# Kernel tuning notes

Hardware: AMD Instinct MI355X
Metric: run time of the kernel (lower is better)

## Reference

```python
import jax, jax.numpy as jnp
import numpy as np

N_NODES = 100000
N_EDGES = 1600000
D_IN = 128
D_OUT = 128


def setup_inputs() -> dict:
    key = jax.random.key(0)
    k1, k2, k3, k4, k5, k6 = jax.random.split(key, 6)
    x = jax.random.normal(k1, (N_NODES, D_IN), dtype=jnp.float32)
    adj_rows = jnp.sort(jax.random.randint(k2, (N_EDGES,), 0, N_NODES, dtype=jnp.int32))
    adj_cols = jax.random.randint(k3, (N_EDGES,), 0, N_NODES, dtype=jnp.int32)
    adj_vals = jax.random.uniform(k4, (N_EDGES,), dtype=jnp.float32)
    weight = jax.random.normal(k5, (D_OUT, D_IN), dtype=jnp.float32) * (1.0 / np.sqrt(D_IN))
    bias = jax.random.normal(k6, (D_OUT,), dtype=jnp.float32) * 0.01
    return {"x": x, "adj_rows": adj_rows, "adj_cols": adj_cols,
            "adj_vals": adj_vals, "weight": weight, "bias": bias}


def reference(x, adj_rows, adj_cols, adj_vals, weight, bias):
    # w_input = inputs @ W.T  -> [N, D_OUT]
    w_input = x @ weight.T
    # SpMM: out[r] = sum_e adj_vals[e] * w_input[cols[e]] for edges with rows[e] == r
    msgs = adj_vals[:, None] * w_input[adj_cols]          # [E, D_OUT]
    agg = jax.ops.segment_sum(msgs, adj_rows, num_segments=N_NODES)
    out = jax.nn.relu(agg + bias)
    return out.astype(jnp.float32)
```

## Files before the change

### kernel.cpp

```cpp
#include <hip/hip_runtime.h>
#include <hip/hip_bf16.h>

#define D 128
#define RPW 2

typedef __attribute__((ext_vector_type(8))) short bf16x8;
typedef __attribute__((ext_vector_type(4))) float f32x4;

__device__ __forceinline__ unsigned short f2bf(float f) {
    union { float f; unsigned u; } uf{f};
    unsigned r = uf.u + 0x7fffu + ((uf.u >> 16) & 1u);
    return (unsigned short)(r >> 16);
}
__device__ __forceinline__ unsigned packcv(float a, float b) {
    __hip_bfloat162 h = __float22bfloat162_rn(make_float2(a, b));
    union { __hip_bfloat162 h; unsigned u; } c{h};
    return c.u;
}
__device__ __forceinline__ float bflo(unsigned u) {
    union { unsigned u; float f; } c{u << 16};
    return c.f;
}
__device__ __forceinline__ float bfhi(unsigned u) {
    union { unsigned u; float f; } c{u & 0xffff0000u};
    return c.f;
}
__device__ __forceinline__ int pc_col(unsigned u) { return (int)(u & 0x1FFFFu); }
__device__ __forceinline__ float pc_val(unsigned u) {
    union { unsigned u; float f; } c{(u >> 1) & 0xFFFF0000u};
    return c.f;
}

#define FMA8(A, vv, u) \
    A[0] = fmaf(vv, bflo(u.x), A[0]); A[1] = fmaf(vv, bfhi(u.x), A[1]); \
    A[2] = fmaf(vv, bflo(u.y), A[2]); A[3] = fmaf(vv, bfhi(u.y), A[3]); \
    A[4] = fmaf(vv, bflo(u.z), A[4]); A[5] = fmaf(vv, bfhi(u.z), A[5]); \
    A[6] = fmaf(vv, bflo(u.w), A[6]); A[7] = fmaf(vv, bfhi(u.w), A[7]);

__global__ __launch_bounds__(256) void build_rowptr(const int* __restrict__ rows,
                                                    const int* __restrict__ cols,
                                                    const float* __restrict__ vals,
                                                    const float* __restrict__ W,
                                                    unsigned short* __restrict__ wbf,
                                                    unsigned* __restrict__ pc,
                                                    int2* __restrict__ rowptr,
                                                    int e, int n) {
    int i = blockIdx.x * 256 + threadIdx.x;
    if (i < D * D) wbf[i] = f2bf(W[i]);
    if (i >= e) return;

    pc[i] = ((unsigned)f2bf(vals[i]) << 17) | (unsigned)cols[i];

    int r = rows[i];
    int prev = (i == 0) ? -1 : rows[i - 1];
    int next = (i == e - 1) ? n : rows[i + 1];
    if (prev != r) {
        rowptr[r].x = i;
        for (int q = prev + 1; q < r; ++q) rowptr[q] = make_int2(i, i);
    }
    if (next != r) {
        rowptr[r].y = i + 1;
        if (i == e - 1)
            for (int q = r + 1; q < n; ++q) rowptr[q] = make_int2(e, e);
    }
}

__global__ __launch_bounds__(256) void gemm_mfma(const float* __restrict__ x,
                                                 const unsigned short* __restrict__ wbf,
                                                 unsigned short* __restrict__ wi,
                                                 int nrows) {
    __shared__ __align__(16) unsigned short Ws[128 * 128];

    const int tid = threadIdx.x;
#pragma unroll
    for (int it = 0; it < 8; ++it) {
        int elem = it * 2048 + tid * 8;
        int r = elem >> 7, k = elem & 127;
        int idx = (r * 128 + k) ^ ((r & 7) << 3);
        *(uint4*)&Ws[idx] = *(const uint4*)(wbf + elem);
    }
    __syncthreads();

    const int lane = tid & 63;
    const int row0 = blockIdx.x * 128 + (tid >> 6) * 32;
    const int lrow = lane & 15;
    const int lk8 = (lane >> 4) * 8;

    bf16x8 xfrag[2][4];
#pragma unroll
    for (int xb = 0; xb < 2; ++xb)
#pragma unroll
        for (int kb = 0; kb < 4; ++kb) {
            int gr = min(row0 + xb * 16 + lrow, nrows - 1);
            const float4* p = (const float4*)(x + (size_t)gr * D + kb * 32 + lk8);
            float4 f0 = p[0], f1 = p[1];
            union { bf16x8 v; unsigned u[4]; } cv;
            cv.u[0] = packcv(f0.x, f0.y);
            cv.u[1] = packcv(f0.z, f0.w);
            cv.u[2] = packcv(f1.x, f1.y);
            cv.u[3] = packcv(f1.z, f1.w);
            xfrag[xb][kb] = cv.v;
        }

    f32x4 acc[2][8];
#pragma unroll
    for (int xb = 0; xb < 2; ++xb)
#pragma unroll
        for (int cb = 0; cb < 8; ++cb)
            acc[xb][cb] = (f32x4){0.f, 0.f, 0.f, 0.f};

#pragma unroll
    for (int cb = 0; cb < 8; ++cb) {
#pragma unroll
        for (int kb = 0; kb < 4; ++kb) {
            int wrow = cb * 16 + lrow;
            int idx = (wrow * 128 + kb * 32 + lk8) ^ ((wrow & 7) << 3);
            bf16x8 wfrag = *(const bf16x8*)&Ws[idx];
            acc[0][cb] = __builtin_amdgcn_mfma_f32_16x16x32_bf16(wfrag, xfrag[0][kb], acc[0][cb], 0, 0, 0);
            acc[1][cb] = __builtin_amdgcn_mfma_f32_16x16x32_bf16(wfrag, xfrag[1][kb], acc[1][cb], 0, 0, 0);
        }
    }

#pragma unroll
    for (int xb = 0; xb < 2; ++xb) {
        int g = row0 + xb * 16 + lrow;
        if (g < nrows) {
#pragma unroll
            for (int cb = 0; cb < 8; ++cb) {
                uint2 o;
                o.x = packcv(acc[xb][cb][0], acc[xb][cb][1]);
                o.y = packcv(acc[xb][cb][2], acc[xb][cb][3]);
                *(uint2*)(wi + (size_t)g * D + cb * 16 + (lane >> 4) * 4) = o;
            }
        }
    }
}

__global__ __launch_bounds__(256) void spmm_relu(const unsigned short* __restrict__ wi,
                                                 const int2* __restrict__ rowptr,
                                                 const unsigned* __restrict__ pc,
                                                 const float* __restrict__ bias,
                                                 float* __restrict__ out,
                                                 int n) {
    const int lane = threadIdx.x & 63;
    const int R0 = (blockIdx.x * 4 + (threadIdx.x >> 6)) * RPW;
    if (R0 >= n) return;
    const int nr = min(RPW, n - R0);

    const int2 rp = rowptr[R0 + min(lane, nr - 1)];
    const int ch = (lane & 15) * 8;
    const int sub = lane >> 4;

    float4 b0 = *(const float4*)(bias + (lane & 15) * 8);
    float4 b1 = *(const float4*)(bias + (lane & 15) * 8 + 4);

    int st = __shfl(rp.x, 0), en = __shfl(rp.y, 0);
    unsigned u = 0;
    { int idx = st + lane; if (idx < en) u = pc[idx]; }

    for (int j = 0; j < nr; ++j) {
        int st_n = 0, en_n = 0; unsigned u_n = 0;
        if (j + 1 < nr) {
            st_n = __shfl(rp.x, j + 1); en_n = __shfl(rp.y, j + 1);
            int idx = st_n + lane; if (idx < en_n) u_n = pc[idx];
        }

        float a0[8] = {0.f, 0.f, 0.f, 0.f, 0.f, 0.f, 0.f, 0.f};
        float a1[8] = {0.f, 0.f, 0.f, 0.f, 0.f, 0.f, 0.f, 0.f};

        const int cnt = min(en - st, 64);
        if (cnt > 0) {
            unsigned mA[4], mB[4];
#pragma unroll
            for (int p = 0; p < 4; ++p) {
                mA[p] = __shfl(u, sub + 4 * p);
                mB[p] = __shfl(u, 16 + sub + 4 * p);
            }
            uint4 uA[4], uB[4];
#pragma unroll
            for (int p = 0; p < 4; ++p) uA[p] = *(const uint4*)(wi + (size_t)pc_col(mA[p]) * D + ch);
#pragma unroll
            for (int p = 0; p < 4; ++p) uB[p] = *(const uint4*)(wi + (size_t)pc_col(mB[p]) * D + ch);
#pragma unroll
            for (int p = 0; p < 4; ++p) {
                FMA8(a0, pc_val(mA[p]), uA[p]);
                FMA8(a1, pc_val(mB[p]), uB[p]);
            }
            for (int E = 32; E < cnt; E += 16) {
#pragma unroll
                for (int p = 0; p < 4; ++p) {
                    unsigned m = __shfl(u, E + sub + 4 * p);
                    uint4 uq = *(const uint4*)(wi + (size_t)pc_col(m) * D + ch);
                    FMA8(a0, pc_val(m), uq);
                }
            }
        }
        for (int base = st + 64; base < en; base += 64) {
            unsigned uu = 0;
            { int idx = base + lane; if (idx < en) uu = pc[idx]; }
            const int cnt2 = min(en - base, 64);
            for (int E = 0; E < cnt2; E += 16) {
#pragma unroll
                for (int p = 0; p < 4; ++p) {
                    unsigned m = __shfl(uu, E + sub + 4 * p);
                    uint4 uq = *(const uint4*)(wi + (size_t)pc_col(m) * D + ch);
                    FMA8(a1, pc_val(m), uq);
                }
            }
        }

        float r8[8];
#pragma unroll
        for (int t = 0; t < 8; ++t) {
            float s = a0[t] + a1[t];
            s += __shfl_xor(s, 16);
            s += __shfl_xor(s, 32);
            r8[t] = s;
        }
        if (lane < 16) {
            float4 o0, o1;
            o0.x = fmaxf(r8[0] + b0.x, 0.f);
            o0.y = fmaxf(r8[1] + b0.y, 0.f);
            o0.z = fmaxf(r8[2] + b0.z, 0.f);
            o0.w = fmaxf(r8[3] + b0.w, 0.f);
            o1.x = fmaxf(r8[4] + b1.x, 0.f);
            o1.y = fmaxf(r8[5] + b1.y, 0.f);
            o1.z = fmaxf(r8[6] + b1.z, 0.f);
            o1.w = fmaxf(r8[7] + b1.w, 0.f);
            *(float4*)(out + (size_t)(R0 + j) * D + lane * 8) = o0;
            *(float4*)(out + (size_t)(R0 + j) * D + lane * 8 + 4) = o1;
        }

        st = st_n; en = en_n; u = u_n;
    }
}

extern "C" void kernel_launch(void* const* d_in, const int* in_sizes, int n_in,
                              void* d_out, int out_size, void* d_ws, size_t ws_size,
                              hipStream_t stream) {
    const float* x        = (const float*)d_in[0];
    const int*   adj_rows = (const int*)d_in[1];
    const int*   adj_cols = (const int*)d_in[2];
    const float* adj_vals = (const float*)d_in[3];
    const float* weight   = (const float*)d_in[4];
    const float* bias     = (const float*)d_in[5];
    float*       out      = (float*)d_out;

    const int n = in_sizes[0] / D;
    const int e = in_sizes[1];

    unsigned short* wi = (unsigned short*)d_ws;
    size_t off = ((size_t)n * D * sizeof(unsigned short) + 255) & ~(size_t)255;
    int2* rowptr = (int2*)((char*)d_ws + off);
    unsigned* pc = (unsigned*)(rowptr + n);
    unsigned short* wbf = (unsigned short*)(pc + e);

    build_rowptr<<<(e + 255) / 256, 256, 0, stream>>>(adj_rows, adj_cols, adj_vals,
                                                      weight, wbf, pc, rowptr, e, n);

    gemm_mfma<<<(n + 127) / 128, 256, 0, stream>>>(x, wbf, wi, n);

    spmm_relu<<<(n + 4 * RPW - 1) / (4 * RPW), 256, 0, stream>>>(
        wi, rowptr, pc, bias, out, n);
}
```

Baseline: 93.96 us.

## Merge rowptr build and GEMM into one launch with in-block weight conversion

Combines the CSR rowptr/packed-edge construction kernel and the MFMA GEMM kernel into a single launch, with disjoint block ranges running each task. Each GEMM block now converts the fp32 weight to bf16 itself instead of reading a pre-converted copy, which removes the dependency between the two stages. This drops one kernel launch and lets the two independent stages overlap on the GPU. In exchange, every GEMM block repeats the weight conversion, and rowptr blocks share the same 32KB shared-memory footprint, which may limit occupancy.

```diff
diff --git a/kernel.cpp b/kernel.cpp
--- a/kernel.cpp
+++ b/kernel.cpp
@@ -37,47 +37,54 @@
     A[4] = fmaf(vv, bflo(u.z), A[4]); A[5] = fmaf(vv, bfhi(u.z), A[5]); \
     A[6] = fmaf(vv, bflo(u.w), A[6]); A[7] = fmaf(vv, bfhi(u.w), A[7]);
 
-__global__ __launch_bounds__(256) void build_rowptr(const int* __restrict__ rows,
-                                                    const int* __restrict__ cols,
-                                                    const float* __restrict__ vals,
-                                                    const float* __restrict__ W,
-                                                    unsigned short* __restrict__ wbf,
-                                                    unsigned* __restrict__ pc,
-                                                    int2* __restrict__ rowptr,
-                                                    int e, int n) {
-    int i = blockIdx.x * 256 + threadIdx.x;
-    if (i < D * D) wbf[i] = f2bf(W[i]);
-    if (i >= e) return;
-
-    pc[i] = ((unsigned)f2bf(vals[i]) << 17) | (unsigned)cols[i];
-
-    int r = rows[i];
-    int prev = (i == 0) ? -1 : rows[i - 1];
-    int next = (i == e - 1) ? n : rows[i + 1];
-    if (prev != r) {
-        rowptr[r].x = i;
-        for (int q = prev + 1; q < r; ++q) rowptr[q] = make_int2(i, i);
-    }
-    if (next != r) {
-        rowptr[r].y = i + 1;
-        if (i == e - 1)
-            for (int q = r + 1; q < n; ++q) rowptr[q] = make_int2(e, e);
-    }
-}
-
-__global__ __launch_bounds__(256) void gemm_mfma(const float* __restrict__ x,
-                                                 const unsigned short* __restrict__ wbf,
-                                                 unsigned short* __restrict__ wi,
-                                                 int nrows) {
+__global__ __launch_bounds__(256) void gemm_and_rowptr(
+        const float* __restrict__ x,
+        const float* __restrict__ W,
+        const int* __restrict__ rows,
+        const int* __restrict__ cols,
+        const float* __restrict__ vals,
+        unsigned short* __restrict__ wi,
+        unsigned* __restrict__ pc,
+        int2* __restrict__ rowptr,
+        int nrows, int e, int gemm_blocks) {
+    const int tid = threadIdx.x;
+
+    if (blockIdx.x >= gemm_blocks) {
+        int i = (blockIdx.x - gemm_blocks) * 256 + tid;
+        if (i >= e) return;
+
+        pc[i] = ((unsigned)f2bf(vals[i]) << 17) | (unsigned)cols[i];
+
+        int r = rows[i];
+        int prev = (i == 0) ? -1 : rows[i - 1];
+        int next = (i == e - 1) ? nrows : rows[i + 1];
+        if (prev != r) {
+            rowptr[r].x = i;
+            for (int q = prev + 1; q < r; ++q) rowptr[q] = make_int2(i, i);
+        }
+        if (next != r) {
+            rowptr[r].y = i + 1;
+            if (i == e - 1)
+                for (int q = r + 1; q < nrows; ++q) rowptr[q] = make_int2(e, e);
+        }
+        return;
+    }
+
     __shared__ __align__(16) unsigned short Ws[128 * 128];
 
-    const int tid = threadIdx.x;
 #pragma unroll
     for (int it = 0; it < 8; ++it) {
         int elem = it * 2048 + tid * 8;
         int r = elem >> 7, k = elem & 127;
         int idx = (r * 128 + k) ^ ((r & 7) << 3);
-        *(uint4*)&Ws[idx] = *(const uint4*)(wbf + elem);
+        const float4* wp = (const float4*)(W + elem);
+        float4 w0 = wp[0], w1 = wp[1];
+        uint4 o;
+        o.x = packcv(w0.x, w0.y);
+        o.y = packcv(w0.z, w0.w);
+        o.z = packcv(w1.x, w1.y);
+        o.w = packcv(w1.z, w1.w);
+        *(uint4*)&Ws[idx] = o;
     }
     __syncthreads();
 
@@ -253,12 +260,13 @@
     size_t off = ((size_t)n * D * sizeof(unsigned short) + 255) & ~(size_t)255;
     int2* rowptr = (int2*)((char*)d_ws + off);
     unsigned* pc = (unsigned*)(rowptr + n);
-    unsigned short* wbf = (unsigned short*)(pc + e);
-
-    build_rowptr<<<(e + 255) / 256, 256, 0, stream>>>(adj_rows, adj_cols, adj_vals,
-                                                      weight, wbf, pc, rowptr, e, n);
-
-    gemm_mfma<<<(n + 127) / 128, 256, 0, stream>>>(x, wbf, wi, n);
+
+    const int gemm_blocks = (n + 127) / 128;
+    const int rp_blocks   = (e + 255) / 256;
+
+    gemm_and_rowptr<<<gemm_blocks + rp_blocks, 256, 0, stream>>>(
+        x, weight, adj_rows, adj_cols, adj_vals, wi, pc, rowptr,
+        n, e, gemm_blocks);
 
     spmm_relu<<<(n + 4 * RPW - 1) / (4 * RPW), 256, 0, stream>>>(
         wi, rowptr, pc, bias, out, n);
```

Measured after the change: 89.44 us. 1.05x faster.
